# Performance work log

Measured on AMD Instinct MI355X. Metric: run time of the kernel, lower is better.

The kernel has to match this reference:

```python
import jax, jax.numpy as jnp
import numpy as np

B, S, IN, OUT = 4, 2048, 4096, 4096


def setup_inputs() -> dict:
    key = jax.random.key(0)
    kx, kw, kb = jax.random.split(key, 3)
    x = jax.random.randint(kx, (B, S, IN), -127, 128, dtype=jnp.int8)
    weight = jax.random.randint(kw, (OUT, IN), -127, 128, dtype=jnp.int8)
    # original module initializes bias to zeros(int32); use random int32 to exercise the add
    bias = jax.random.randint(kb, (1, OUT), -1000, 1000, dtype=jnp.int32)
    return {"x": x, "weight": weight, "bias": bias}


def reference(x, weight, bias):
    x_shape = x.shape
    x2 = x.reshape(-1, x_shape[-1])  # [tokens, IN], int8
    # dot_general with preferred_element_type=int32 -> int8 inputs, int32 accumulate
    y = jax.lax.dot_general(
        x2, weight,
        dimension_numbers=(((1,), (1,)), ((), ())),
        preferred_element_type=jnp.int32,
    )  # [tokens, OUT] int32
    y = y + bias  # broadcast [1, OUT] int32
    return y.reshape(*x_shape[:-1], -1)
```

## Files before the change

### kernel.cpp

```cpp
#include <hip/hip_runtime.h>
#include <stdint.h>

#define M_TOT 8192
#define N_TOT 4096
#define K_TOT 4096

typedef int v4i  __attribute__((ext_vector_type(4)));
typedef int v16i __attribute__((ext_vector_type(16)));

__device__ __forceinline__ void gload_lds16(const void* g, void* l) {
    __builtin_amdgcn_global_load_lds(
        (const __attribute__((address_space(1))) unsigned int*)g,
        (__attribute__((address_space(3))) unsigned int*)l,
        16, 0, 0);
}

__global__ __launch_bounds__(256) void pack_i32_to_i8(
        const int4* __restrict__ src, int* __restrict__ dst, int n4) {
    const int idx = blockIdx.x * 256 + threadIdx.x;
    if (idx >= n4) return;
    const int4 a = src[idx];
    dst[idx] = (a.x & 255) | ((a.y & 255) << 8) | ((a.z & 255) << 16) | (a.w << 24);
}

__global__ __launch_bounds__(64, 1) void i8gemm_bias(
        const signed char* __restrict__ x,
        const signed char* __restrict__ w,
        const int* __restrict__ bias,
        int* __restrict__ out) {
    __shared__ __align__(16) signed char la[128 * 64];
    __shared__ __align__(16) signed char lb[128 * 64];

    const int lane = threadIdx.x;
    const int l31  = lane & 31;
    const int kh   = lane >> 5;
    const int bm0  = blockIdx.y * 128;
    const int bn0  = blockIdx.x * 128;

    int bv[4];
#pragma unroll
    for (int j = 0; j < 4; ++j) bv[j] = bias[bn0 + j * 32 + l31];
    v16i acc[4][4];
#pragma unroll
    for (int i = 0; i < 4; ++i)
#pragma unroll
        for (int j = 0; j < 4; ++j)
#pragma unroll
            for (int r = 0; r < 16; ++r) acc[i][j][r] = bv[j];

    const int fc = (lane & 3) ^ ((lane >> 3) & 3);
    const signed char* pa = x + (long)(bm0 + (lane >> 2)) * K_TOT + fc * 16;
    const signed char* pb = w + (long)(bn0 + (lane >> 2)) * K_TOT + fc * 16;

    const int swr = (l31 >> 1) & 3;

    for (int kt = 0; kt < K_TOT / 64; ++kt) {
        const long k0 = (long)kt * 64;
        __syncthreads();
#pragma unroll
        for (int i = 0; i < 8; ++i) {
            gload_lds16(pa + k0 + (long)i * 16 * K_TOT, la + i * 1024);
            gload_lds16(pb + k0 + (long)i * 16 * K_TOT, lb + i * 1024);
        }
        __syncthreads();

#pragma unroll
        for (int kk = 0; kk < 2; ++kk) {
            const int cs = ((kk * 2 + kh) ^ swr) * 16;
            v4i af[4], bf[4];
#pragma unroll
            for (int i = 0; i < 4; ++i) {
                af[i] = *(const v4i*)(la + (i * 32 + l31) * 64 + cs);
                bf[i] = *(const v4i*)(lb + (i * 32 + l31) * 64 + cs);
            }
#pragma unroll
            for (int i = 0; i < 4; ++i)
#pragma unroll
                for (int j = 0; j < 4; ++j)
                    acc[i][j] = __builtin_amdgcn_mfma_i32_32x32x32_i8(
                        af[i], bf[j], acc[i][j], 0, 0, 0);
        }
    }

#pragma unroll
    for (int i = 0; i < 4; ++i) {
        const int mbase = bm0 + i * 32 + 4 * kh;
#pragma unroll
        for (int j = 0; j < 4; ++j) {
            const int n = bn0 + j * 32 + l31;
#pragma unroll
            for (int r = 0; r < 16; ++r) {
                const int m = mbase + (r & 3) + 8 * (r >> 2);
                out[(long)m * N_TOT + n] = acc[i][j][r];
            }
        }
    }
}

extern "C" void kernel_launch(void* const* d_in, const int* in_sizes, int n_in,
                              void* d_out, int out_size, void* d_ws, size_t ws_size,
                              hipStream_t stream) {
    const int* x32  = (const int*)d_in[0];
    const int* w32  = (const int*)d_in[1];
    const int* bias = (const int*)d_in[2];
    int*       out  = (int*)d_out;

    signed char* xp = (signed char*)d_ws;
    signed char* wp = (signed char*)d_ws + (size_t)M_TOT * K_TOT;

    const int n4x = (M_TOT * K_TOT) / 4;
    const int n4w = (N_TOT * K_TOT) / 4;
    pack_i32_to_i8<<<n4x / 256, 256, 0, stream>>>((const int4*)x32, (int*)xp, n4x);
    pack_i32_to_i8<<<n4w / 256, 256, 0, stream>>>((const int4*)w32, (int*)wp, n4w);

    dim3 grid(N_TOT / 128, M_TOT / 128);
    i8gemm_bias<<<grid, 64, 0, stream>>>(xp, wp, bias, out);
}
```

Baseline: 415.2 us.

## Double-buffer LDS tiles to overlap global loads with MFMA compute

The GEMM kernel now keeps two LDS buffers per operand and prefetches the next K tile directly into the spare buffer while the current tile's fragments feed the MFMAs. A vmcnt wait replaces the pair of barriers, and sched_barriers fix the order of loads, prefetch and MFMA. The aim is to hide global-load latency in a one-wave block that previously stalled on every tile. The pack kernels also handle four int4 elements per thread with a quarter of the blocks, dropping the bounds check. LDS use doubles, and the single-wave design is what makes skipping the barrier safe.

```diff
diff --git a/kernel.cpp b/kernel.cpp
--- a/kernel.cpp
+++ b/kernel.cpp
@@ -15,12 +15,17 @@
         16, 0, 0);
 }
 
+#define WAIT_VMCNT0() __builtin_amdgcn_s_waitcnt(0x0f70)
+
 __global__ __launch_bounds__(256) void pack_i32_to_i8(
         const int4* __restrict__ src, int* __restrict__ dst, int n4) {
-    const int idx = blockIdx.x * 256 + threadIdx.x;
-    if (idx >= n4) return;
-    const int4 a = src[idx];
-    dst[idx] = (a.x & 255) | ((a.y & 255) << 8) | ((a.z & 255) << 16) | (a.w << 24);
+    int idx = blockIdx.x * 1024 + threadIdx.x;
+#pragma unroll
+    for (int u = 0; u < 4; ++u, idx += 256) {
+        const int4 a = src[idx];
+        dst[idx] = (a.x & 255) | ((a.y & 255) << 8) |
+                   ((a.z & 255) << 16) | (a.w << 24);
+    }
 }
 
 __global__ __launch_bounds__(64, 1) void i8gemm_bias(
@@ -28,8 +33,8 @@
         const signed char* __restrict__ w,
         const int* __restrict__ bias,
         int* __restrict__ out) {
-    __shared__ __align__(16) signed char la[128 * 64];
-    __shared__ __align__(16) signed char lb[128 * 64];
+    __shared__ __align__(16) signed char la[2][128 * 64];
+    __shared__ __align__(16) signed char lb[2][128 * 64];
 
     const int lane = threadIdx.x;
     const int l31  = lane & 31;
@@ -54,32 +59,52 @@
 
     const int swr = (l31 >> 1) & 3;
 
+#pragma unroll
+    for (int i = 0; i < 8; ++i) {
+        gload_lds16(pa + (long)i * 16 * K_TOT, &la[0][i * 1024]);
+        gload_lds16(pb + (long)i * 16 * K_TOT, &lb[0][i * 1024]);
+    }
+
     for (int kt = 0; kt < K_TOT / 64; ++kt) {
-        const long k0 = (long)kt * 64;
-        __syncthreads();
-#pragma unroll
-        for (int i = 0; i < 8; ++i) {
-            gload_lds16(pa + k0 + (long)i * 16 * K_TOT, la + i * 1024);
-            gload_lds16(pb + k0 + (long)i * 16 * K_TOT, lb + i * 1024);
-        }
-        __syncthreads();
+        const int cur = kt & 1;
+        const signed char* lac = la[cur];
+        const signed char* lbc = lb[cur];
 
+        WAIT_VMCNT0();
+        __builtin_amdgcn_sched_barrier(0);
+
+        v4i af[2][4], bf[2][4];
 #pragma unroll
         for (int kk = 0; kk < 2; ++kk) {
             const int cs = ((kk * 2 + kh) ^ swr) * 16;
-            v4i af[4], bf[4];
 #pragma unroll
             for (int i = 0; i < 4; ++i) {
-                af[i] = *(const v4i*)(la + (i * 32 + l31) * 64 + cs);
-                bf[i] = *(const v4i*)(lb + (i * 32 + l31) * 64 + cs);
+                af[kk][i] = *(const v4i*)(lac + (i * 32 + l31) * 64 + cs);
+                bf[kk][i] = *(const v4i*)(lbc + (i * 32 + l31) * 64 + cs);
             }
+        }
+        __builtin_amdgcn_sched_barrier(0);
+
+        if (kt + 1 < K_TOT / 64) {
+            const long k0 = (long)(kt + 1) * 64;
+            signed char* lan = la[cur ^ 1];
+            signed char* lbn = lb[cur ^ 1];
+#pragma unroll
+            for (int i = 0; i < 8; ++i) {
+                gload_lds16(pa + k0 + (long)i * 16 * K_TOT, lan + i * 1024);
+                gload_lds16(pb + k0 + (long)i * 16 * K_TOT, lbn + i * 1024);
+            }
+        }
+        __builtin_amdgcn_sched_barrier(0);
+
+#pragma unroll
+        for (int kk = 0; kk < 2; ++kk)
 #pragma unroll
             for (int i = 0; i < 4; ++i)
 #pragma unroll
                 for (int j = 0; j < 4; ++j)
                     acc[i][j] = __builtin_amdgcn_mfma_i32_32x32x32_i8(
-                        af[i], bf[j], acc[i][j], 0, 0, 0);
-        }
+                        af[kk][i], bf[kk][j], acc[i][j], 0, 0, 0);
     }
 
 #pragma unroll
@@ -110,8 +135,8 @@
 
     const int n4x = (M_TOT * K_TOT) / 4;
     const int n4w = (N_TOT * K_TOT) / 4;
-    pack_i32_to_i8<<<n4x / 256, 256, 0, stream>>>((const int4*)x32, (int*)xp, n4x);
-    pack_i32_to_i8<<<n4w / 256, 256, 0, stream>>>((const int4*)w32, (int*)wp, n4w);
+    pack_i32_to_i8<<<n4x / 1024, 256, 0, stream>>>((const int4*)x32, (int*)xp, n4x);
+    pack_i32_to_i8<<<n4w / 1024, 256, 0, stream>>>((const int4*)w32, (int*)wp, n4w);
 
     dim3 grid(N_TOT / 128, M_TOT / 128);
     i8gemm_bias<<<grid, 64, 0, stream>>>(xp, wp, bias, out);
```

Result: no change. 412.3 us (-0.7%).
